# Kernel tuning notes

Measured on AMD Instinct MI355X. Metric: run time of the kernel, lower is better.

Reference implementation:

```python
import jax, jax.numpy as jnp
import numpy as np

# Model dims (match init_kwargs / input_specs)
T, N, E, F_IN, F_OUT, BW = 16, 50000, 131072, 64, 64, 3


def setup_inputs() -> dict:
    key = jax.random.key(0)
    ks = jax.random.split(key, 6)
    x = jax.random.normal(ks[0], (T, N, F_IN), dtype=jnp.float32)
    M = jax.random.normal(ks[1], (T, T), dtype=jnp.float32)
    adj_rows = jax.random.randint(ks[2], (T, E), 0, N, dtype=jnp.int32)
    adj_cols = jax.random.randint(ks[3], (T, E), 0, N, dtype=jnp.int32)
    adj_vals = jax.random.uniform(ks[4], (T, E), dtype=jnp.float32)
    lim = float(np.sqrt(6.0 / (F_IN + F_OUT)))  # xavier_uniform
    weight = jax.random.uniform(ks[5], (F_IN, F_OUT), minval=-lim, maxval=lim, dtype=jnp.float32)
    return {"x": x, "M": M, "adj_vals": adj_vals, "weight": weight,
            "adj_rows": adj_rows, "adj_cols": adj_cols}


def _spmm(vals, rows, cols, x):
    # COO sparse [N,N] @ dense [N,F]: gather source rows, scatter-add to dest rows.
    return jax.ops.segment_sum(vals[:, None] * x[cols], rows, num_segments=x.shape[0])


def reference(x, M, adj_vals, weight, adj_rows, adj_cols):
    Tn, Nn, F = x.shape
    # Xt = M @ X (full M, as in compute_AtXt)
    Xt = (M @ x.reshape(Tn, -1)).reshape(Tn, Nn, F)
    k_idx = jnp.arange(Tn)
    AtXt = jnp.zeros((Tn, Nn, F), dtype=x.dtype)
    # Banded combination: At[k] = sum_{d=0}^{BW-1, k-d>=0} M[k, k-d] * A[k-d]
    # so At[k] @ Xt[k] = sum_d M[k,k-d] * (A[k-d] @ Xt[k])  -- avoids materializing At.
    for d in range(BW):
        j = k_idx - d
        valid = j >= 0
        jc = jnp.maximum(j, 0)
        w = jnp.where(valid, M[k_idx, jc], 0.0)  # [T] banded weights
        contrib = jax.vmap(_spmm)(adj_vals[jc], adj_rows[jc], adj_cols[jc], Xt)  # [T,N,F]
        AtXt = AtXt + w[:, None, None] * contrib
    # dropout is identity in eval mode; final dense projection
    return AtXt @ weight  # [T, N, F_OUT]
```

## Files before the change

kernel.cpp:

```cpp
#include <hip/hip_runtime.h>

#define TT 16
#define NN 50000
#define FF 64
#define EE 131072
#define NEDGE (TT*EE)
#define RPB 32
#define NRANGE ((NN + RPB - 1) / RPB)
#define NSUB 8
#define BCAP 256
#define NBUCK (NRANGE*NSUB)
#define SLOTS (NSUB*BCAP)
#define EMAX 1791
#define TAILI (EMAX*2)

typedef __attribute__((ext_vector_type(8))) short bf16x8;
typedef __attribute__((ext_vector_type(4))) short bf16x4;
typedef __attribute__((ext_vector_type(4))) float f32x4;

__device__ __forceinline__ unsigned pack2bf(float a, float b) {
    unsigned ua = __float_as_uint(a) + 0x8000u;
    unsigned ub = __float_as_uint(b) + 0x8000u;
    return __builtin_amdgcn_perm(ub, ua, 0x07060302u);
}
__device__ __forceinline__ float lo16f(unsigned u) { return __uint_as_float(u << 16); }
__device__ __forceinline__ float hi16f(unsigned u) { return __uint_as_float(u & 0xFFFF0000u); }

union U8 { unsigned u[4]; bf16x8 v; };
union U4 { unsigned u[2]; bf16x4 v; };

__device__ __forceinline__ f32x4 mfma16x16x16bf16(bf16x4 a, bf16x4 b, f32x4 c) {
#if __has_builtin(__builtin_amdgcn_mfma_f32_16x16x16bf16_1k)
    return __builtin_amdgcn_mfma_f32_16x16x16bf16_1k(a, b, c, 0, 0, 0);
#elif __has_builtin(__builtin_amdgcn_mfma_f32_16x16x16_bf16)
    return __builtin_amdgcn_mfma_f32_16x16x16_bf16(a, b, c, 0, 0, 0);
#else
    f32x4 d;
    asm volatile("v_mfma_f32_16x16x16_bf16 %0, %1, %2, %3\n\ts_nop 7\n\ts_nop 7"
                 : "=&v"(d) : "v"(a), "v"(b), "v"(c));
    return d;
#endif
}

__global__ __launch_bounds__(256) void k1_proj_mix(
    const float* __restrict__ x, const float* __restrict__ M,
    const float* __restrict__ W, unsigned short* __restrict__ Yt)
{
    const int tid  = threadIdx.x;
    const int wid  = tid >> 6;
    const int lane = tid & 63;
    const int col  = lane & 15;
    const int grp  = lane >> 4;

    bf16x8 bw[2][4];
#pragma unroll
    for (int q = 0; q < 2; ++q)
#pragma unroll
        for (int t = 0; t < 4; ++t) {
            U8 w8;
#pragma unroll
            for (int p = 0; p < 4; ++p)
                w8.u[p] = pack2bf(W[(q*32 + grp*8 + 2*p)*FF + t*16 + col],
                                  W[(q*32 + grp*8 + 2*p + 1)*FF + t*16 + col]);
            bw[q][t] = w8.v;
        }

    U4 m4;
    m4.u[0] = pack2bf(M[col*16 + grp*4 + 0], M[col*16 + grp*4 + 1]);
    m4.u[1] = pack2bf(M[col*16 + grp*4 + 2], M[col*16 + grp*4 + 3]);
    const bf16x4 mf = m4.v;

    const f32x4 zero = {0.f, 0.f, 0.f, 0.f};
    const int nwaves = gridDim.x * 4;

    for (int node = blockIdx.x*4 + wid; node < NN; node += nwaves) {
        const float* xb = x + (size_t)col*NN*FF + (size_t)node*FF + grp*8;
        float4 v0 = *reinterpret_cast<const float4*>(xb);
        float4 v1 = *reinterpret_cast<const float4*>(xb + 4);
        float4 v2 = *reinterpret_cast<const float4*>(xb + 32);
        float4 v3 = *reinterpret_cast<const float4*>(xb + 36);
        U8 a0, a1;
        a0.u[0] = pack2bf(v0.x, v0.y); a0.u[1] = pack2bf(v0.z, v0.w);
        a0.u[2] = pack2bf(v1.x, v1.y); a0.u[3] = pack2bf(v1.z, v1.w);
        a1.u[0] = pack2bf(v2.x, v2.y); a1.u[1] = pack2bf(v2.z, v2.w);
        a1.u[2] = pack2bf(v3.x, v3.y); a1.u[3] = pack2bf(v3.z, v3.w);

        f32x4 acc[4];
#pragma unroll
        for (int t = 0; t < 4; ++t) acc[t] = zero;
#pragma unroll
        for (int t = 0; t < 4; ++t)
            acc[t] = __builtin_amdgcn_mfma_f32_16x16x32_bf16(a0.v, bw[0][t], acc[t], 0, 0, 0);
#pragma unroll
        for (int t = 0; t < 4; ++t)
            acc[t] = __builtin_amdgcn_mfma_f32_16x16x32_bf16(a1.v, bw[1][t], acc[t], 0, 0, 0);

#pragma unroll
        for (int t = 0; t < 4; ++t) {
            U4 pb;
            pb.u[0] = pack2bf(acc[t][0], acc[t][1]);
            pb.u[1] = pack2bf(acc[t][2], acc[t][3]);
            f32x4 y = mfma16x16x16bf16(pb.v, mf, zero);
            uint2 st;
            st.x = pack2bf(y[0], y[1]);
            st.y = pack2bf(y[2], y[3]);
            *reinterpret_cast<uint2*>(Yt + (size_t)node*1024 + col*64 + t*16 + grp*4) = st;
        }
    }
}

__global__ __launch_bounds__(256) void append_kernel(
    const int* __restrict__ rows, const int* __restrict__ cols,
    const float* __restrict__ vals, int* __restrict__ bcnt,
    int2* __restrict__ btmp)
{
    const int i = blockIdx.x*256 + threadIdx.x;
    const int r = rows[i];
    const int j = i >> 17;
    const int b = (r >> 5)*NSUB + (blockIdx.x & 7);
    const int pos = atomicAdd(&bcnt[b], 1);
    if (pos < BCAP) {
        int2 e;
        e.x = cols[i] | (((r & 31)*16 + j) << 16);
        e.y = __float_as_int(vals[i]);
        btmp[(size_t)b*BCAP + pos] = e;
    }
}

__global__ __launch_bounds__(256) void sort_kernel(
    const int* __restrict__ bcnt, int2* __restrict__ btmp)
{
    __shared__ int2 sbuf[SLOTS];
    __shared__ int scnt[512], soff[512], scur[512], pscan[256];

    const int tid = threadIdx.x;
    const int blk = blockIdx.x;
    int2* region = btmp + (size_t)blk*SLOTS;

    scnt[tid] = 0; scnt[tid + 256] = 0;
    __syncthreads();

    int bc[NSUB]; int2 ent[NSUB];
#pragma unroll
    for (int s = 0; s < NSUB; ++s) {
        int c = bcnt[blk*NSUB + s];
        bc[s] = c < BCAP ? c : BCAP;
    }
#pragma unroll
    for (int s = 0; s < NSUB; ++s)
        if (tid < bc[s]) {
            ent[s] = region[s*BCAP + tid];
            atomicAdd(&scnt[((unsigned)ent[s].x) >> 16], 1);
        }
    __syncthreads();

    const int a0 = scnt[2*tid], a1 = scnt[2*tid + 1];
    const int ps = a0 + a1;
    pscan[tid] = ps;
    __syncthreads();
    for (int o = 1; o < 256; o <<= 1) {
        int v = (tid >= o) ? pscan[tid - o] : 0;
        __syncthreads();
        pscan[tid] += v;
        __syncthreads();
    }
    const int excl = pscan[tid] - ps;
    soff[2*tid] = excl;      soff[2*tid + 1] = excl + a0;
    scur[2*tid] = excl;      scur[2*tid + 1] = excl + a0;
    __syncthreads();

#pragma unroll
    for (int s = 0; s < NSUB; ++s)
        if (tid < bc[s]) {
            const int key = ((unsigned)ent[s].x) >> 16;
            const int pos = atomicAdd(&scur[key], 1);
            int2 se; se.x = ent[s].x & 0xFFFF; se.y = ent[s].y;
            sbuf[pos] = se;
        }
    __syncthreads();

    const int total = soff[511] + scnt[511];
    const int lim = total < EMAX ? total : EMAX;
    for (int i = tid; i < lim; i += 256) region[i] = sbuf[i];
    int* tail = (int*)region + TAILI;
    tail[tid] = soff[tid];
    tail[tid + 256] = soff[tid + 256];
    if (tid == 0) tail[512] = lim;
}

template<int J>
__device__ __forceinline__ void k2_batch(int p0, int nj, int sbase, int esub, int fq,
    const int2* eb, const unsigned short* __restrict__ Yt,
    const float* __restrict__ M, f32x4* acc)
{
    const int p = p0 + esub;
    const bool act = p < nj;
    const int li = act ? (sbase + p) : 0;
    const int2 ent = eb[li];
    const float v = act ? __int_as_float(ent.y) : 0.f;
    const int node = act ? ent.x : 0;
    const unsigned short* yb = Yt + (size_t)node*1024 + J*64 + fq*4;
    {
        const uint2 uv = *reinterpret_cast<const uint2*>(yb);
        const float wv = M[J*17] * v;
        acc[J][0] = fmaf(wv, lo16f(uv.x), acc[J][0]);
        acc[J][1] = fmaf(wv, hi16f(uv.x), acc[J][1]);
        acc[J][2] = fmaf(wv, lo16f(uv.y), acc[J][2]);
        acc[J][3] = fmaf(wv, hi16f(uv.y), acc[J][3]);
    }
    if constexpr (J < 15) {
        const uint2 uv = *reinterpret_cast<const uint2*>(yb + 64);
        const float wv = M[J*17 + 16] * v;
        acc[J+1][0] = fmaf(wv, lo16f(uv.x), acc[J+1][0]);
        acc[J+1][1] = fmaf(wv, hi16f(uv.x), acc[J+1][1]);
        acc[J+1][2] = fmaf(wv, lo16f(uv.y), acc[J+1][2]);
        acc[J+1][3] = fmaf(wv, hi16f(uv.y), acc[J+1][3]);
    }
    if constexpr (J < 14) {
        const uint2 uv = *reinterpret_cast<const uint2*>(yb + 128);
        const float wv = M[J*17 + 32] * v;
        acc[J+2][0] = fmaf(wv, lo16f(uv.x), acc[J+2][0]);
        acc[J+2][1] = fmaf(wv, hi16f(uv.x), acc[J+2][1]);
        acc[J+2][2] = fmaf(wv, lo16f(uv.y), acc[J+2][2]);
        acc[J+2][3] = fmaf(wv, hi16f(uv.y), acc[J+2][3]);
    }
}

__global__ __launch_bounds__(256) void k2_gather(
    const unsigned short* __restrict__ Yt, const float* __restrict__ M,
    const int2* __restrict__ btmp, float* __restrict__ out)
{
    __shared__ int2 ebuf[4][128];
    const int tid  = threadIdx.x;
    const int wid  = tid >> 6;
    const int lane = tid & 63;
    const int esub = lane >> 4;
    const int fq   = lane & 15;
    const int r   = blockIdx.x*4 + wid;
    const int blk = r >> 5;
    const int rl  = r & 31;

    const int2* region = btmp + (size_t)blk*SLOTS;
    const int* tail = (const int*)region + TAILI;
    int o_l = 0;
    if (lane < 17) o_l = tail[rl*16 + lane];
    int off[17];
#pragma unroll
    for (int j = 0; j < 17; ++j) off[j] = __builtin_amdgcn_readlane(o_l, j);
    int ntot = off[16] - off[0];
    ntot = ntot < 128 ? ntot : 128;
    const int2* rowsrc = region + off[0];

    int2* eb = ebuf[wid];
    if (lane < ntot)      eb[lane]      = rowsrc[lane];
    if (lane + 64 < ntot) eb[lane + 64] = rowsrc[lane + 64];

    int c[16], sb[16];
#pragma unroll
    for (int j = 0; j < 16; ++j) {
        c[j]  = off[j+1] - off[j];
        sb[j] = off[j] - off[0];
    }

    f32x4 acc[16];
#pragma unroll
    for (int k = 0; k < 16; ++k) acc[k] = (f32x4){0.f, 0.f, 0.f, 0.f};

#define P1(J) k2_batch<J>(0, c[J], sb[J], esub, fq, eb, Yt, M, acc);
    P1(0)  P1(1)  P1(2)  P1(3)  P1(4)  P1(5)  P1(6)  P1(7)
    P1(8)  P1(9)  P1(10) P1(11) P1(12) P1(13) P1(14) P1(15)
#undef P1
#define P2(J) for (int p0 = 4; p0 < c[J]; p0 += 4) \
        k2_batch<J>(p0, c[J], sb[J], esub, fq, eb, Yt, M, acc);
    P2(0)  P2(1)  P2(2)  P2(3)  P2(4)  P2(5)  P2(6)  P2(7)
    P2(8)  P2(9)  P2(10) P2(11) P2(12) P2(13) P2(14) P2(15)
#undef P2

#pragma unroll
    for (int k = 0; k < 16; ++k) {
#pragma unroll
        for (int u = 0; u < 4; ++u) {
            acc[k][u] += __shfl_xor(acc[k][u], 16);
            acc[k][u] += __shfl_xor(acc[k][u], 32);
        }
    }
    if (esub == 0) {
#pragma unroll
        for (int k = 0; k < 16; ++k) {
            float4 res; res.x = acc[k][0]; res.y = acc[k][1];
            res.z = acc[k][2]; res.w = acc[k][3];
            *reinterpret_cast<float4*>(out + ((size_t)k*NN + r)*FF + fq*4) = res;
        }
    }
}

extern "C" void kernel_launch(void* const* d_in, const int* in_sizes, int n_in,
                              void* d_out, int out_size, void* d_ws, size_t ws_size,
                              hipStream_t stream) {
    (void)in_sizes; (void)n_in; (void)out_size; (void)ws_size;
    const float* x     = (const float*)d_in[0];
    const float* M     = (const float*)d_in[1];
    const float* avals = (const float*)d_in[2];
    const float* W     = (const float*)d_in[3];
    const int*   arows = (const int*)d_in[4];
    const int*   acols = (const int*)d_in[5];
    float* out = (float*)d_out;

    char* ws = (char*)d_ws;
    size_t o = 0;
    unsigned short* Yt = (unsigned short*)(ws + o); o += (size_t)TT*NN*FF*2;
    o = (o + 255) & ~(size_t)255;
    int* bcnt = (int*)(ws + o); o += (size_t)NBUCK*4;  o = (o + 255) & ~(size_t)255;
    int2* btmp = (int2*)(ws + o);

    hipMemsetAsync(bcnt, 0, (size_t)NBUCK*4, stream);
    hipLaunchKernelGGL(k1_proj_mix, dim3(2048), dim3(256), 0, stream, x, M, W, Yt);
    hipLaunchKernelGGL(append_kernel, dim3(NEDGE/256), dim3(256), 0, stream,
                       arows, acols, avals, bcnt, btmp);
    hipLaunchKernelGGL(sort_kernel, dim3(NRANGE), dim3(256), 0, stream, bcnt, btmp);
    hipLaunchKernelGGL(k2_gather, dim3(12500), dim3(256), 0, stream, Yt, M, btmp, out);
}
```

Baseline: 362.4 us.

## Split gather rows across two waves by output time range, add nontemporal loads/stores

The gather kernel now gives each destination row to two waves. Each wave accumulates only 8 of the 16 output time slices, covering source slices 0-7 or 6-15, which halves the accumulator registers and doubles the grid. A launch-bounds occupancy hint is added. Nontemporal loads and stores are used for streamed inputs, edge buffers and the output. The cost is redundant Yt reads for the overlapping slices 6-7, and the shared edge buffer is now capped at 96 entries per wave.

```diff
diff --git a/kernel.cpp b/kernel.cpp
--- a/kernel.cpp
+++ b/kernel.cpp
@@ -17,6 +17,8 @@
 typedef __attribute__((ext_vector_type(8))) short bf16x8;
 typedef __attribute__((ext_vector_type(4))) short bf16x4;
 typedef __attribute__((ext_vector_type(4))) float f32x4;
+typedef __attribute__((ext_vector_type(2))) int   i32x2;
+typedef __attribute__((ext_vector_type(2))) unsigned u32x2;
 
 __device__ __forceinline__ unsigned pack2bf(float a, float b) {
     unsigned ua = __float_as_uint(a) + 0x8000u;
@@ -75,15 +77,15 @@
 
     for (int node = blockIdx.x*4 + wid; node < NN; node += nwaves) {
         const float* xb = x + (size_t)col*NN*FF + (size_t)node*FF + grp*8;
-        float4 v0 = *reinterpret_cast<const float4*>(xb);
-        float4 v1 = *reinterpret_cast<const float4*>(xb + 4);
-        float4 v2 = *reinterpret_cast<const float4*>(xb + 32);
-        float4 v3 = *reinterpret_cast<const float4*>(xb + 36);
+        f32x4 v0 = __builtin_nontemporal_load(reinterpret_cast<const f32x4*>(xb));
+        f32x4 v1 = __builtin_nontemporal_load(reinterpret_cast<const f32x4*>(xb + 4));
+        f32x4 v2 = __builtin_nontemporal_load(reinterpret_cast<const f32x4*>(xb + 32));
+        f32x4 v3 = __builtin_nontemporal_load(reinterpret_cast<const f32x4*>(xb + 36));
         U8 a0, a1;
-        a0.u[0] = pack2bf(v0.x, v0.y); a0.u[1] = pack2bf(v0.z, v0.w);
-        a0.u[2] = pack2bf(v1.x, v1.y); a0.u[3] = pack2bf(v1.z, v1.w);
-        a1.u[0] = pack2bf(v2.x, v2.y); a1.u[1] = pack2bf(v2.z, v2.w);
-        a1.u[2] = pack2bf(v3.x, v3.y); a1.u[3] = pack2bf(v3.z, v3.w);
+        a0.u[0] = pack2bf(v0[0], v0[1]); a0.u[1] = pack2bf(v0[2], v0[3]);
+        a0.u[2] = pack2bf(v1[0], v1[1]); a0.u[3] = pack2bf(v1[2], v1[3]);
+        a1.u[0] = pack2bf(v2[0], v2[1]); a1.u[1] = pack2bf(v2[2], v2[3]);
+        a1.u[2] = pack2bf(v3[0], v3[1]); a1.u[3] = pack2bf(v3[2], v3[3]);
 
         f32x4 acc[4];
 #pragma unroll
@@ -101,10 +103,10 @@
             pb.u[0] = pack2bf(acc[t][0], acc[t][1]);
             pb.u[1] = pack2bf(acc[t][2], acc[t][3]);
             f32x4 y = mfma16x16x16bf16(pb.v, mf, zero);
-            uint2 st;
-            st.x = pack2bf(y[0], y[1]);
-            st.y = pack2bf(y[2], y[3]);
-            *reinterpret_cast<uint2*>(Yt + (size_t)node*1024 + col*64 + t*16 + grp*4) = st;
+            u32x2 st;
+            st[0] = pack2bf(y[0], y[1]);
+            st[1] = pack2bf(y[2], y[3]);
+            *reinterpret_cast<u32x2*>(Yt + (size_t)node*1024 + col*64 + t*16 + grp*4) = st;
         }
     }
 }
@@ -112,35 +114,35 @@
 __global__ __launch_bounds__(256) void append_kernel(
     const int* __restrict__ rows, const int* __restrict__ cols,
     const float* __restrict__ vals, int* __restrict__ bcnt,
-    int2* __restrict__ btmp)
+    i32x2* __restrict__ btmp)
 {
     const int i = blockIdx.x*256 + threadIdx.x;
-    const int r = rows[i];
+    const int r = __builtin_nontemporal_load(rows + i);
     const int j = i >> 17;
     const int b = (r >> 5)*NSUB + (blockIdx.x & 7);
     const int pos = atomicAdd(&bcnt[b], 1);
     if (pos < BCAP) {
-        int2 e;
-        e.x = cols[i] | (((r & 31)*16 + j) << 16);
-        e.y = __float_as_int(vals[i]);
+        i32x2 e;
+        e[0] = __builtin_nontemporal_load(cols + i) | (((r & 31)*16 + j) << 16);
+        e[1] = __float_as_int(__builtin_nontemporal_load(vals + i));
         btmp[(size_t)b*BCAP + pos] = e;
     }
 }
 
 __global__ __launch_bounds__(256) void sort_kernel(
-    const int* __restrict__ bcnt, int2* __restrict__ btmp)
-{
-    __shared__ int2 sbuf[SLOTS];
+    const int* __restrict__ bcnt, i32x2* __restrict__ btmp)
+{
+    __shared__ i32x2 sbuf[SLOTS];
     __shared__ int scnt[512], soff[512], scur[512], pscan[256];
 
     const int tid = threadIdx.x;
     const int blk = blockIdx.x;
-    int2* region = btmp + (size_t)blk*SLOTS;
+    i32x2* region = btmp + (size_t)blk*SLOTS;
 
     scnt[tid] = 0; scnt[tid + 256] = 0;
     __syncthreads();
 
-    int bc[NSUB]; int2 ent[NSUB];
+    int bc[NSUB]; i32x2 ent[NSUB];
 #pragma unroll
     for (int s = 0; s < NSUB; ++s) {
         int c = bcnt[blk*NSUB + s];
@@ -150,7 +152,7 @@
     for (int s = 0; s < NSUB; ++s)
         if (tid < bc[s]) {
             ent[s] = region[s*BCAP + tid];
-            atomicAdd(&scnt[((unsigned)ent[s].x) >> 16], 1);
+            atomicAdd(&scnt[((unsigned)ent[s][0]) >> 16], 1);
         }
     __syncthreads();
 
@@ -172,9 +174,9 @@
 #pragma unroll
     for (int s = 0; s < NSUB; ++s)
         if (tid < bc[s]) {
-            const int key = ((unsigned)ent[s].x) >> 16;
+            const int key = ((unsigned)ent[s][0]) >> 16;
             const int pos = atomicAdd(&scur[key], 1);
-            int2 se; se.x = ent[s].x & 0xFFFF; se.y = ent[s].y;
+            i32x2 se; se[0] = ent[s][0] & 0xFFFF; se[1] = ent[s][1];
             sbuf[pos] = se;
         }
     __syncthreads();
@@ -188,96 +190,96 @@
     if (tid == 0) tail[512] = lim;
 }
 
-template<int J>
+template<int J, int KLO, int KHI>
 __device__ __forceinline__ void k2_batch(int p0, int nj, int sbase, int esub, int fq,
-    const int2* eb, const unsigned short* __restrict__ Yt,
+    const i32x2* eb, const unsigned short* __restrict__ Yt,
     const float* __restrict__ M, f32x4* acc)
 {
     const int p = p0 + esub;
     const bool act = p < nj;
     const int li = act ? (sbase + p) : 0;
-    const int2 ent = eb[li];
-    const float v = act ? __int_as_float(ent.y) : 0.f;
-    const int node = act ? ent.x : 0;
-    const unsigned short* yb = Yt + (size_t)node*1024 + J*64 + fq*4;
-    {
-        const uint2 uv = *reinterpret_cast<const uint2*>(yb);
-        const float wv = M[J*17] * v;
-        acc[J][0] = fmaf(wv, lo16f(uv.x), acc[J][0]);
-        acc[J][1] = fmaf(wv, hi16f(uv.x), acc[J][1]);
-        acc[J][2] = fmaf(wv, lo16f(uv.y), acc[J][2]);
-        acc[J][3] = fmaf(wv, hi16f(uv.y), acc[J][3]);
-    }
-    if constexpr (J < 15) {
-        const uint2 uv = *reinterpret_cast<const uint2*>(yb + 64);
-        const float wv = M[J*17 + 16] * v;
-        acc[J+1][0] = fmaf(wv, lo16f(uv.x), acc[J+1][0]);
-        acc[J+1][1] = fmaf(wv, hi16f(uv.x), acc[J+1][1]);
-        acc[J+1][2] = fmaf(wv, lo16f(uv.y), acc[J+1][2]);
-        acc[J+1][3] = fmaf(wv, hi16f(uv.y), acc[J+1][3]);
-    }
-    if constexpr (J < 14) {
-        const uint2 uv = *reinterpret_cast<const uint2*>(yb + 128);
-        const float wv = M[J*17 + 32] * v;
-        acc[J+2][0] = fmaf(wv, lo16f(uv.x), acc[J+2][0]);
-        acc[J+2][1] = fmaf(wv, hi16f(uv.x), acc[J+2][1]);
-        acc[J+2][2] = fmaf(wv, lo16f(uv.y), acc[J+2][2]);
-        acc[J+2][3] = fmaf(wv, hi16f(uv.y), acc[J+2][3]);
-    }
-}
-
-__global__ __launch_bounds__(256) void k2_gather(
+    const i32x2 ent = eb[li];
+    const float v = act ? __int_as_float(ent[1]) : 0.f;
+    const int node = act ? ent[0] : 0;
+    const unsigned short* yb = Yt + (size_t)node*1024 + fq*4;
+#pragma unroll
+    for (int d = 0; d < 3; ++d) {
+        if (J + d >= KLO && J + d <= KHI && J + d < 16) {
+            const u32x2 uv = *reinterpret_cast<const u32x2*>(yb + (J + d)*64);
+            const float wv = M[(J + d)*16 + J] * v;
+            acc[J + d - KLO][0] = fmaf(wv, lo16f(uv[0]), acc[J + d - KLO][0]);
+            acc[J + d - KLO][1] = fmaf(wv, hi16f(uv[0]), acc[J + d - KLO][1]);
+            acc[J + d - KLO][2] = fmaf(wv, lo16f(uv[1]), acc[J + d - KLO][2]);
+            acc[J + d - KLO][3] = fmaf(wv, hi16f(uv[1]), acc[J + d - KLO][3]);
+        }
+    }
+}
+
+__global__ __launch_bounds__(256, 8) void k2_gather(
     const unsigned short* __restrict__ Yt, const float* __restrict__ M,
-    const int2* __restrict__ btmp, float* __restrict__ out)
-{
-    __shared__ int2 ebuf[4][128];
+    const i32x2* __restrict__ btmp, float* __restrict__ out)
+{
+    __shared__ i32x2 ebuf[4][96];
     const int tid  = threadIdx.x;
     const int wid  = tid >> 6;
     const int lane = tid & 63;
     const int esub = lane >> 4;
     const int fq   = lane & 15;
-    const int r   = blockIdx.x*4 + wid;
+    const int rown = wid >> 1;
+    const int half = wid & 1;
+    const int r   = blockIdx.x*2 + rown;
     const int blk = r >> 5;
     const int rl  = r & 31;
 
-    const int2* region = btmp + (size_t)blk*SLOTS;
+    const i32x2* region = btmp + (size_t)blk*SLOTS;
     const int* tail = (const int*)region + TAILI;
     int o_l = 0;
-    if (lane < 17) o_l = tail[rl*16 + lane];
+    if (lane < 17) o_l = __builtin_nontemporal_load(tail + rl*16 + lane);
     int off[17];
 #pragma unroll
     for (int j = 0; j < 17; ++j) off[j] = __builtin_amdgcn_readlane(o_l, j);
-    int ntot = off[16] - off[0];
-    ntot = ntot < 128 ? ntot : 128;
-    const int2* rowsrc = region + off[0];
-
-    int2* eb = ebuf[wid];
-    if (lane < ntot)      eb[lane]      = rowsrc[lane];
-    if (lane + 64 < ntot) eb[lane + 64] = rowsrc[lane + 64];
+
+    const int jlo = half ? 6 : 0;
+    const int jhi = half ? 15 : 7;
+    int ntot = off[jhi + 1] - off[jlo];
+    ntot = ntot < 96 ? ntot : 96;
+    const i32x2* rowsrc = region + off[jlo];
+
+    i32x2* eb = ebuf[wid];
+    if (lane < ntot)      eb[lane]      = __builtin_nontemporal_load(rowsrc + lane);
+    if (lane + 64 < ntot) eb[lane + 64] = __builtin_nontemporal_load(rowsrc + lane + 64);
 
     int c[16], sb[16];
 #pragma unroll
     for (int j = 0; j < 16; ++j) {
         c[j]  = off[j+1] - off[j];
-        sb[j] = off[j] - off[0];
-    }
-
-    f32x4 acc[16];
-#pragma unroll
-    for (int k = 0; k < 16; ++k) acc[k] = (f32x4){0.f, 0.f, 0.f, 0.f};
-
-#define P1(J) k2_batch<J>(0, c[J], sb[J], esub, fq, eb, Yt, M, acc);
-    P1(0)  P1(1)  P1(2)  P1(3)  P1(4)  P1(5)  P1(6)  P1(7)
-    P1(8)  P1(9)  P1(10) P1(11) P1(12) P1(13) P1(14) P1(15)
+        sb[j] = off[j] - off[jlo];
+    }
+
+    f32x4 acc[8];
+#pragma unroll
+    for (int k = 0; k < 8; ++k) acc[k] = (f32x4){0.f, 0.f, 0.f, 0.f};
+
+    if (half == 0) {
+#define P1(J) k2_batch<J,0,7>(0, c[J], sb[J], esub, fq, eb, Yt, M, acc);
+        P1(0) P1(1) P1(2) P1(3) P1(4) P1(5) P1(6) P1(7)
 #undef P1
 #define P2(J) for (int p0 = 4; p0 < c[J]; p0 += 4) \
-        k2_batch<J>(p0, c[J], sb[J], esub, fq, eb, Yt, M, acc);
-    P2(0)  P2(1)  P2(2)  P2(3)  P2(4)  P2(5)  P2(6)  P2(7)
-    P2(8)  P2(9)  P2(10) P2(11) P2(12) P2(13) P2(14) P2(15)
+            k2_batch<J,0,7>(p0, c[J], sb[J], esub, fq, eb, Yt, M, acc);
+        P2(0) P2(1) P2(2) P2(3) P2(4) P2(5) P2(6) P2(7)
 #undef P2
-
-#pragma unroll
-    for (int k = 0; k < 16; ++k) {
+    } else {
+#define P1(J) k2_batch<J,8,15>(0, c[J], sb[J], esub, fq, eb, Yt, M, acc);
+        P1(6) P1(7) P1(8) P1(9) P1(10) P1(11) P1(12) P1(13) P1(14) P1(15)
+#undef P1
+#define P2(J) for (int p0 = 4; p0 < c[J]; p0 += 4) \
+            k2_batch<J,8,15>(p0, c[J], sb[J], esub, fq, eb, Yt, M, acc);
+        P2(6) P2(7) P2(8) P2(9) P2(10) P2(11) P2(12) P2(13) P2(14) P2(15)
+#undef P2
+    }
+
+#pragma unroll
+    for (int k = 0; k < 8; ++k) {
 #pragma unroll
         for (int u = 0; u < 4; ++u) {
             acc[k][u] += __shfl_xor(acc[k][u], 16);
@@ -285,11 +287,11 @@
         }
     }
     if (esub == 0) {
-#pragma unroll
-        for (int k = 0; k < 16; ++k) {
-            float4 res; res.x = acc[k][0]; res.y = acc[k][1];
-            res.z = acc[k][2]; res.w = acc[k][3];
-            *reinterpret_cast<float4*>(out + ((size_t)k*NN + r)*FF + fq*4) = res;
+        const int kbase = half*8;
+#pragma unroll
+        for (int k = 0; k < 8; ++k) {
+            __builtin_nontemporal_store(acc[k],
+                reinterpret_cast<f32x4*>(out + ((size_t)(kbase + k)*NN + r)*FF + fq*4));
         }
     }
 }
@@ -311,12 +313,12 @@
     unsigned short* Yt = (unsigned short*)(ws + o); o += (size_t)TT*NN*FF*2;
     o = (o + 255) & ~(size_t)255;
     int* bcnt = (int*)(ws + o); o += (size_t)NBUCK*4;  o = (o + 255) & ~(size_t)255;
-    int2* btmp = (int2*)(ws + o);
-
-    hipMemsetAsync(bcnt, 0, (size_t)NBUCK*4, stream);
+    i32x2* btmp = (i32x2*)(ws + o);
+
+    (void)hipMemsetAsync(bcnt, 0, (size_t)NBUCK*4, stream);
     hipLaunchKernelGGL(k1_proj_mix, dim3(2048), dim3(256), 0, stream, x, M, W, Yt);
     hipLaunchKernelGGL(append_kernel, dim3(NEDGE/256), dim3(256), 0, stream,
                        arows, acols, avals, bcnt, btmp);
     hipLaunchKernelGGL(sort_kernel, dim3(NRANGE), dim3(256), 0, stream, bcnt, btmp);
-    hipLaunchKernelGGL(k2_gather, dim3(12500), dim3(256), 0, stream, Yt, M, btmp, out);
-}
+    hipLaunchKernelGGL(k2_gather, dim3(25000), dim3(256), 0, stream, Yt, M, btmp, out);
+}
```

New measurement: 503.9 us. +39.0%, slower.
